# Kernel tuning notes

Measured on AMD Instinct MI355X. Metric: run time of the kernel, lower is better.

The kernel has to match this reference:

```python
import jax, jax.numpy as jnp
import numpy as np
from jax import lax

S = 1024  # input_size
G = 10    # grid_size
F = 5     # fiter_size -> 11x11 gaussian kernel
B = 8
C = 3


def _gauss(size, fwhm):
    x = np.arange(size, dtype=np.float64)
    y = x[:, None]
    c = size // 2
    g = np.exp(-4 * np.log(2) * ((x - c) ** 2 + (y - c) ** 2) / fwhm ** 2)
    return (g / g.sum()).astype(np.float32)


def setup_inputs() -> dict:
    key = jax.random.key(0)
    k1, k2, k3 = jax.random.split(key, 3)
    x = jax.random.normal(k1, (B, C, S, S), dtype=jnp.float32)
    offset_x = jax.random.normal(k2, (B, 1, G, G), dtype=jnp.float32)
    offset_y = jax.random.normal(k3, (B, 1, G, G), dtype=jnp.float32)
    weight = jnp.asarray(_gauss(2 * F + 1, F))[None, None]  # [1,1,11,11]
    return {"x": x, "offset_x": offset_x, "offset_y": offset_y,
            "weight": weight, "max_move": 50}


def reference(x, offset_x, offset_y, weight, max_move):
    max_offset = 2.0 * max_move / S

    def smooth(o):  # replication pad + 11x11 gaussian conv + scale + clamp
        p = jnp.pad(o, ((0, 0), (0, 0), (F, F), (F, F)), mode="edge")
        c = lax.conv_general_dilated(p, weight, (1, 1), "VALID",
                                     dimension_numbers=("NCHW", "OIHW", "NCHW"))
        return jnp.clip(c * max_offset, -max_offset, max_offset)

    g = jnp.concatenate([smooth(offset_x), smooth(offset_y)], axis=1)  # [B,2,G,G]

    # bilinear upsample G -> S (align_corners=False, like F.interpolate)
    src = jnp.maximum((jnp.arange(S, dtype=jnp.float32) + 0.5) * (G / S) - 0.5, 0.0)
    i0 = jnp.minimum(jnp.floor(src).astype(jnp.int32), G - 1)
    i1 = jnp.minimum(i0 + 1, G - 1)
    w = src - i0.astype(jnp.float32)
    g = g[:, :, i0, :] * (1 - w)[None, None, :, None] + g[:, :, i1, :] * w[None, None, :, None]
    g = g[:, :, :, i0] * (1 - w) + g[:, :, :, i1] * w  # [B,2,S,S]

    # P basis: channel 0 = x coord, channel 1 = y coord, scaled to [-1,1]
    lin = jnp.arange(S, dtype=jnp.float32) / (S - 1.0)
    P = jnp.stack([jnp.broadcast_to(lin[None, :], (S, S)),
                   jnp.broadcast_to(lin[:, None], (S, S))]) * 2.0 - 1.0
    grid = jnp.clip(g + P, -1.0, 1.0).transpose(0, 2, 3, 1)  # [B,S,S,2] (x,y)

    def gs(img, gr):  # grid_sample bilinear, zeros padding, align_corners=False
        ix = ((gr[..., 0] + 1.0) * S - 1.0) / 2.0
        iy = ((gr[..., 1] + 1.0) * S - 1.0) / 2.0
        x0 = jnp.floor(ix).astype(jnp.int32); x1 = x0 + 1
        y0 = jnp.floor(iy).astype(jnp.int32); y1 = y0 + 1
        wx = ix - x0.astype(ix.dtype)
        wy = iy - y0.astype(iy.dtype)

        def corner(yy, xx, wt):
            v = img[:, jnp.clip(yy, 0, S - 1), jnp.clip(xx, 0, S - 1)]  # [C,S,S]
            m = ((yy >= 0) & (yy < S) & (xx >= 0) & (xx < S)).astype(img.dtype)
            return v * (m * wt)

        return (corner(y0, x0, (1 - wy) * (1 - wx)) + corner(y0, x1, (1 - wy) * wx)
                + corner(y1, x0, wy * (1 - wx)) + corner(y1, x1, wy * wx))

    return jax.vmap(gs)(x, grid)
```

## Files before the change

### kernel.cpp

```cpp
#include <hip/hip_runtime.h>

#define SS 1024
#define GG 10
#define FF 5
#define BB 8
#define CC 3

__global__ __launch_bounds__(256) void rds_smooth_kernel(
    const float* __restrict__ ox, const float* __restrict__ oy,
    const float* __restrict__ w, const void* __restrict__ max_move_p,
    float* __restrict__ gs)
{
    int idx = blockIdx.x * 256 + threadIdx.x;
    if (idx >= BB * 2 * GG * GG) return;
    int j  = idx % GG;
    int i  = (idx / GG) % GG;
    int ch = (idx / (GG * GG)) % 2;
    int b  = idx / (2 * GG * GG);

    const float* o = (ch == 0 ? ox : oy) + b * GG * GG;

    int mi = *(const int*)max_move_p;
    float mv = (mi >= -100000 && mi <= 100000) ? (float)mi : __int_as_float(mi);
    float max_offset = 2.0f * mv / (float)SS;

    float acc = 0.0f;
    for (int u = 0; u < 2 * FF + 1; ++u) {
        int yy = min(max(i + u - FF, 0), GG - 1);
        for (int v = 0; v < 2 * FF + 1; ++v) {
            int xx = min(max(j + v - FF, 0), GG - 1);
            acc += o[yy * GG + xx] * w[u * (2 * FF + 1) + v];
        }
    }
    acc *= max_offset;
    acc = fminf(fmaxf(acc, -max_offset), max_offset);
    gs[idx] = acc;
}

__global__ __launch_bounds__(256) void rds_deform_kernel(
    const float* __restrict__ x, const float* __restrict__ gs,
    float* __restrict__ out)
{
    int bx   = blockIdx.x;
    int xseg = bx & 3;
    int y    = (bx >> 2) & (SS - 1);
    int b    = bx >> 12;
    int xc   = xseg * 256 + threadIdx.x;

    __shared__ float g0[GG * GG];
    __shared__ float g1[GG * GG];
    if (threadIdx.x < GG * GG) {
        g0[threadIdx.x] = gs[(b * 2 + 0) * GG * GG + threadIdx.x];
        g1[threadIdx.x] = gs[(b * 2 + 1) * GG * GG + threadIdx.x];
    }
    __syncthreads();

    const float GdS = (float)GG / (float)SS;

    float sy  = fmaxf(((float)y + 0.5f) * GdS - 0.5f, 0.0f);
    int   i0y = min((int)floorf(sy), GG - 1);
    int   i1y = min(i0y + 1, GG - 1);
    float wyu = sy - (float)i0y;

    float sx  = fmaxf(((float)xc + 0.5f) * GdS - 0.5f, 0.0f);
    int   i0x = min((int)floorf(sx), GG - 1);
    int   i1x = min(i0x + 1, GG - 1);
    float wxu = sx - (float)i0x;

    float a00 = g0[i0y * GG + i0x], a10 = g0[i1y * GG + i0x];
    float a01 = g0[i0y * GG + i1x], a11 = g0[i1y * GG + i1x];
    float gxv = (a00 * (1.0f - wyu) + a10 * wyu) * (1.0f - wxu)
              + (a01 * (1.0f - wyu) + a11 * wyu) * wxu;

    float b00 = g1[i0y * GG + i0x], b10 = g1[i1y * GG + i0x];
    float b01 = g1[i0y * GG + i1x], b11 = g1[i1y * GG + i1x];
    float gyv = (b00 * (1.0f - wyu) + b10 * wyu) * (1.0f - wxu)
              + (b01 * (1.0f - wyu) + b11 * wyu) * wxu;

    float px = (float)xc * (2.0f / (float)(SS - 1)) - 1.0f;
    float py = (float)y  * (2.0f / (float)(SS - 1)) - 1.0f;

    float gr0 = fminf(fmaxf(gxv + px, -1.0f), 1.0f);
    float gr1 = fminf(fmaxf(gyv + py, -1.0f), 1.0f);

    float ix = ((gr0 + 1.0f) * (float)SS - 1.0f) * 0.5f;
    float iy = ((gr1 + 1.0f) * (float)SS - 1.0f) * 0.5f;

    int   x0 = (int)floorf(ix);
    int   x1 = x0 + 1;
    int   y0 = (int)floorf(iy);
    int   y1 = y0 + 1;
    float wx = ix - (float)x0;
    float wy = iy - (float)y0;

    float m_x0 = (x0 >= 0 && x0 < SS) ? 1.0f : 0.0f;
    float m_x1 = (x1 >= 0 && x1 < SS) ? 1.0f : 0.0f;
    float m_y0 = (y0 >= 0 && y0 < SS) ? 1.0f : 0.0f;
    float m_y1 = (y1 >= 0 && y1 < SS) ? 1.0f : 0.0f;

    float w00 = (1.0f - wy) * (1.0f - wx) * m_y0 * m_x0;
    float w01 = (1.0f - wy) * wx          * m_y0 * m_x1;
    float w10 = wy          * (1.0f - wx) * m_y1 * m_x0;
    float w11 = wy          * wx          * m_y1 * m_x1;

    int cx0 = min(max(x0, 0), SS - 1);
    int cx1 = min(max(x1, 0), SS - 1);
    int cy0 = min(max(y0, 0), SS - 1);
    int cy1 = min(max(y1, 0), SS - 1);

    const float* xb = x + (size_t)b * CC * SS * SS;
    size_t o00 = (size_t)cy0 * SS + cx0;
    size_t o01 = (size_t)cy0 * SS + cx1;
    size_t o10 = (size_t)cy1 * SS + cx0;
    size_t o11 = (size_t)cy1 * SS + cx1;

    #pragma unroll
    for (int c = 0; c < CC; ++c) {
        const float* img = xb + (size_t)c * SS * SS;
        float v = img[o00] * w00 + img[o01] * w01
                + img[o10] * w10 + img[o11] * w11;
        out[(((size_t)b * CC + c) * SS + y) * SS + xc] = v;
    }
}

extern "C" void kernel_launch(void* const* d_in, const int* in_sizes, int n_in,
                              void* d_out, int out_size, void* d_ws, size_t ws_size,
                              hipStream_t stream) {
    const float* x        = (const float*)d_in[0];
    const float* offset_x = (const float*)d_in[1];
    const float* offset_y = (const float*)d_in[2];
    const float* weight   = (const float*)d_in[3];
    const void*  max_move = d_in[4];
    float* out = (float*)d_out;
    float* gs  = (float*)d_ws;

    int n1 = BB * 2 * GG * GG;
    rds_smooth_kernel<<<(n1 + 255) / 256, 256, 0, stream>>>(
        offset_x, offset_y, weight, max_move, gs);

    int nblocks = BB * SS * (SS / 256);
    rds_deform_kernel<<<nblocks, 256, 0, stream>>>(x, gs, out);
}
```

Measured before the change: 215.7 us.

## Process four pixels per thread with row-precomputed grid and vector nontemporal stores

The deform kernel now gives each block a full output row and each thread four adjacent pixels. Per block, the vertical interpolation of the coarse offset grid is done once into a small shared row instead of loading the whole 10x10 grid. Output is written with 128-bit nontemporal stores, and offsets use 32-bit ints. The aim is fewer blocks, less redundant interpolation work and wider stores, at the cost of more registers per thread and less parallelism per thread for hiding gather latency.

```diff
diff --git a/kernel.cpp b/kernel.cpp
--- a/kernel.cpp
+++ b/kernel.cpp
@@ -5,6 +5,9 @@
 #define FF 5
 #define BB 8
 #define CC 3
+#define KK (2 * FF + 1)
+
+typedef float f32x4 __attribute__((ext_vector_type(4)));
 
 __global__ __launch_bounds__(256) void rds_smooth_kernel(
     const float* __restrict__ ox, const float* __restrict__ oy,
@@ -25,11 +28,11 @@
     float max_offset = 2.0f * mv / (float)SS;
 
     float acc = 0.0f;
-    for (int u = 0; u < 2 * FF + 1; ++u) {
+    for (int u = 0; u < KK; ++u) {
         int yy = min(max(i + u - FF, 0), GG - 1);
-        for (int v = 0; v < 2 * FF + 1; ++v) {
+        for (int v = 0; v < KK; ++v) {
             int xx = min(max(j + v - FF, 0), GG - 1);
-            acc += o[yy * GG + xx] * w[u * (2 * FF + 1) + v];
+            acc += o[yy * GG + xx] * w[u * KK + v];
         }
     }
     acc *= max_offset;
@@ -41,85 +44,97 @@
     const float* __restrict__ x, const float* __restrict__ gs,
     float* __restrict__ out)
 {
-    int bx   = blockIdx.x;
-    int xseg = bx & 3;
-    int y    = (bx >> 2) & (SS - 1);
-    int b    = bx >> 12;
-    int xc   = xseg * 256 + threadIdx.x;
+    int bx  = blockIdx.x;
+    int y   = bx & (SS - 1);
+    int b   = bx >> 10;
+    int tid = threadIdx.x;
 
-    __shared__ float g0[GG * GG];
-    __shared__ float g1[GG * GG];
-    if (threadIdx.x < GG * GG) {
-        g0[threadIdx.x] = gs[(b * 2 + 0) * GG * GG + threadIdx.x];
-        g1[threadIdx.x] = gs[(b * 2 + 1) * GG * GG + threadIdx.x];
-    }
-    __syncthreads();
+    __shared__ float row0[GG];
+    __shared__ float row1[GG];
 
     const float GdS = (float)GG / (float)SS;
 
     float sy  = fmaxf(((float)y + 0.5f) * GdS - 0.5f, 0.0f);
-    int   i0y = min((int)floorf(sy), GG - 1);
+    int   i0y = min((int)sy, GG - 1);
     int   i1y = min(i0y + 1, GG - 1);
     float wyu = sy - (float)i0y;
 
-    float sx  = fmaxf(((float)xc + 0.5f) * GdS - 0.5f, 0.0f);
-    int   i0x = min((int)floorf(sx), GG - 1);
-    int   i1x = min(i0x + 1, GG - 1);
-    float wxu = sx - (float)i0x;
+    if (tid < 2 * GG) {
+        int ch = tid / GG;
+        int j  = tid - ch * GG;
+        const float* gb = gs + (b * 2 + ch) * GG * GG;
+        float v = gb[i0y * GG + j] * (1.0f - wyu) + gb[i1y * GG + j] * wyu;
+        (ch ? row1 : row0)[j] = v;
+    }
+    __syncthreads();
 
-    float a00 = g0[i0y * GG + i0x], a10 = g0[i1y * GG + i0x];
-    float a01 = g0[i0y * GG + i1x], a11 = g0[i1y * GG + i1x];
-    float gxv = (a00 * (1.0f - wyu) + a10 * wyu) * (1.0f - wxu)
-              + (a01 * (1.0f - wyu) + a11 * wyu) * wxu;
+    float py = (float)y * (2.0f / (float)(SS - 1)) - 1.0f;
 
-    float b00 = g1[i0y * GG + i0x], b10 = g1[i1y * GG + i0x];
-    float b01 = g1[i0y * GG + i1x], b11 = g1[i1y * GG + i1x];
-    float gyv = (b00 * (1.0f - wyu) + b10 * wyu) * (1.0f - wxu)
-              + (b01 * (1.0f - wyu) + b11 * wyu) * wxu;
+    int   o00[4], o01[4], o10[4], o11[4];
+    float w00[4], w01[4], w10[4], w11[4];
 
-    float px = (float)xc * (2.0f / (float)(SS - 1)) - 1.0f;
-    float py = (float)y  * (2.0f / (float)(SS - 1)) - 1.0f;
+    #pragma unroll
+    for (int p = 0; p < 4; ++p) {
+        int xc = (tid << 2) + p;
 
-    float gr0 = fminf(fmaxf(gxv + px, -1.0f), 1.0f);
-    float gr1 = fminf(fmaxf(gyv + py, -1.0f), 1.0f);
+        float sx  = fmaxf(((float)xc + 0.5f) * GdS - 0.5f, 0.0f);
+        int   i0x = min((int)sx, GG - 1);
+        int   i1x = min(i0x + 1, GG - 1);
+        float wxu = sx - (float)i0x;
 
-    float ix = ((gr0 + 1.0f) * (float)SS - 1.0f) * 0.5f;
-    float iy = ((gr1 + 1.0f) * (float)SS - 1.0f) * 0.5f;
+        float gxv = row0[i0x] + wxu * (row0[i1x] - row0[i0x]);
+        float gyv = row1[i0x] + wxu * (row1[i1x] - row1[i0x]);
 
-    int   x0 = (int)floorf(ix);
-    int   x1 = x0 + 1;
-    int   y0 = (int)floorf(iy);
-    int   y1 = y0 + 1;
-    float wx = ix - (float)x0;
-    float wy = iy - (float)y0;
+        float pxc = (float)xc * (2.0f / (float)(SS - 1)) - 1.0f;
+        float gr0 = fminf(fmaxf(gxv + pxc, -1.0f), 1.0f);
+        float gr1 = fminf(fmaxf(gyv + py,  -1.0f), 1.0f);
 
-    float m_x0 = (x0 >= 0 && x0 < SS) ? 1.0f : 0.0f;
-    float m_x1 = (x1 >= 0 && x1 < SS) ? 1.0f : 0.0f;
-    float m_y0 = (y0 >= 0 && y0 < SS) ? 1.0f : 0.0f;
-    float m_y1 = (y1 >= 0 && y1 < SS) ? 1.0f : 0.0f;
+        float ix = gr0 * 512.0f + 511.5f;
+        float iy = gr1 * 512.0f + 511.5f;
 
-    float w00 = (1.0f - wy) * (1.0f - wx) * m_y0 * m_x0;
-    float w01 = (1.0f - wy) * wx          * m_y0 * m_x1;
-    float w10 = wy          * (1.0f - wx) * m_y1 * m_x0;
-    float w11 = wy          * wx          * m_y1 * m_x1;
+        int   x0 = (int)floorf(ix);
+        int   x1 = x0 + 1;
+        int   y0 = (int)floorf(iy);
+        int   y1 = y0 + 1;
+        float wx = ix - (float)x0;
+        float wy = iy - (float)y0;
 
-    int cx0 = min(max(x0, 0), SS - 1);
-    int cx1 = min(max(x1, 0), SS - 1);
-    int cy0 = min(max(y0, 0), SS - 1);
-    int cy1 = min(max(y1, 0), SS - 1);
+        float mx0 = ((unsigned)x0 < (unsigned)SS) ? 1.0f : 0.0f;
+        float mx1 = ((unsigned)x1 < (unsigned)SS) ? 1.0f : 0.0f;
+        float my0 = ((unsigned)y0 < (unsigned)SS) ? 1.0f : 0.0f;
+        float my1 = ((unsigned)y1 < (unsigned)SS) ? 1.0f : 0.0f;
+
+        w00[p] = (1.0f - wy) * (1.0f - wx) * my0 * mx0;
+        w01[p] = (1.0f - wy) * wx          * my0 * mx1;
+        w10[p] = wy          * (1.0f - wx) * my1 * mx0;
+        w11[p] = wy          * wx          * my1 * mx1;
+
+        int cx0 = min(max(x0, 0), SS - 1);
+        int cx1 = min(max(x1, 0), SS - 1);
+        int cy0 = min(max(y0, 0), SS - 1);
+        int cy1 = min(max(y1, 0), SS - 1);
+
+        o00[p] = cy0 * SS + cx0;
+        o01[p] = cy0 * SS + cx1;
+        o10[p] = cy1 * SS + cx0;
+        o11[p] = cy1 * SS + cx1;
+    }
 
     const float* xb = x + (size_t)b * CC * SS * SS;
-    size_t o00 = (size_t)cy0 * SS + cx0;
-    size_t o01 = (size_t)cy0 * SS + cx1;
-    size_t o10 = (size_t)cy1 * SS + cx0;
-    size_t o11 = (size_t)cy1 * SS + cx1;
+    size_t obase = (((size_t)b * CC) * SS + y) * SS + (tid << 2);
 
     #pragma unroll
     for (int c = 0; c < CC; ++c) {
         const float* img = xb + (size_t)c * SS * SS;
-        float v = img[o00] * w00 + img[o01] * w01
-                + img[o10] * w10 + img[o11] * w11;
-        out[(((size_t)b * CC + c) * SS + y) * SS + xc] = v;
+        float v[4];
+        #pragma unroll
+        for (int p = 0; p < 4; ++p) {
+            v[p] = img[o00[p]] * w00[p] + img[o01[p]] * w01[p]
+                 + img[o10[p]] * w10[p] + img[o11[p]] * w11[p];
+        }
+        f32x4 r = { v[0], v[1], v[2], v[3] };
+        f32x4* op = (f32x4*)(out + obase + (size_t)c * SS * SS);
+        __builtin_nontemporal_store(r, op);
     }
 }
 
@@ -138,6 +153,6 @@
     rds_smooth_kernel<<<(n1 + 255) / 256, 256, 0, stream>>>(
         offset_x, offset_y, weight, max_move, gs);
 
-    int nblocks = BB * SS * (SS / 256);
+    int nblocks = BB * SS;
     rds_deform_kernel<<<nblocks, 256, 0, stream>>>(x, gs, out);
 }
```

After: 244.0 us. +13.1%, slower.
